# Optimization experiments

Hardware: AMD Instinct MI355X
Metric: run time of the kernel (lower is better)

The kernel has to match this reference:

```python
import jax, jax.numpy as jnp
import numpy as np

HIDDEN = 256        # hidden width of the dynamics MLP
N_ODE_STEPS = 2     # fixed-step RK4 steps over t_sim = [0, 1] per block


def setup_inputs() -> dict:
    key = jax.random.key(0)
    ks = jax.random.split(key, 8)
    S, B, N, d, p, block = 2, 8, 2048, 64, 32, 8
    s = jax.random.normal(ks[0], (S, B, N, d), jnp.float32)
    # strictly increasing time grid so delta = diff(t) > 0
    dt_raw = jax.random.uniform(ks[1], (S, B, block + 1), jnp.float32)
    t = jnp.cumsum(0.05 + 0.1 * dt_raw, axis=2)
    Phi = jax.random.normal(ks[2], (S, B, N, p), jnp.float32)
    b = 0.1 * jax.random.normal(ks[3], (S, B, N, d), jnp.float32)
    W1 = jax.random.normal(ks[4], (d + p, HIDDEN), jnp.float32) / np.sqrt(d + p).astype(np.float32)
    b1 = jnp.zeros((HIDDEN,), jnp.float32)
    W2 = jax.random.normal(ks[5], (HIDDEN, d), jnp.float32) / np.sqrt(HIDDEN).astype(np.float32)
    b2 = jnp.zeros((d,), jnp.float32)
    return dict(s=s, t=t, Phi=Phi, b=b, W1=W1, b1=b1, W2=W2, b2=b2)


def _dyn(x, Phi, b, W1, b1, W2, b2):
    # f(t, x, Phi, b): MLP over per-node latent + spatial features, plus forcing b.
    h = jnp.tanh(jnp.einsum('sbnf,fh->sbnh', jnp.concatenate([x, Phi], axis=-1), W1) + b1)
    return jnp.einsum('sbnh,hd->sbnd', h, W2) + b2 + b


def reference(s, t, Phi, b, W1, b1, W2, b2):
    S, B, N, d = s.shape
    block = t.shape[2] - 1
    delta = jnp.diff(t, axis=2)                      # (S, B, block)
    deltas = jnp.moveaxis(delta, 2, 0)[..., None, None]  # (block, S, B, 1, 1)
    dt = 1.0 / N_ODE_STEPS

    def g(x, dlt):
        # scaled dynamics: f(t, x, Phi, b) * delta  (time-rescaled to [0, 1])
        return _dyn(x, Phi, b, W1, b1, W2, b2) * dlt

    def block_step(x, dlt):
        def rk4(x, _):
            k1 = g(x, dlt)
            k2 = g(x + 0.5 * dt * k1, dlt)
            k3 = g(x + 0.5 * dt * k2, dlt)
            k4 = g(x + dt * k3, dlt)
            return x + (dt / 6.0) * (k1 + 2.0 * k2 + 2.0 * k3 + k4), None
        x, _ = jax.lax.scan(rk4, x, None, length=N_ODE_STEPS)
        return x, x

    _, s_stack = jax.lax.scan(block_step, s, deltas)  # (block, S, B, N, d)
    # 'S B block N d -> S (B block) N d'
    return jnp.moveaxis(s_stack, 0, 2).reshape(S, B * block, N, d)
```

## Files before the change

### kernel.cpp

```cpp
#include <hip/hip_runtime.h>

typedef short  short8   __attribute__((ext_vector_type(8)));
typedef float  floatx4  __attribute__((ext_vector_type(4)));
typedef unsigned int uintx2 __attribute__((ext_vector_type(2)));

#define LOG2E_X2 2.8853900817779268f

__device__ __forceinline__ float tanh_pre(float y) {
    float e = __builtin_amdgcn_exp2f(y);
    return 1.0f - 2.0f * __builtin_amdgcn_rcpf(1.0f + e);
}

__device__ __forceinline__ unsigned short bf16rne(float f) {
    unsigned u = __float_as_uint(f);
    u += 0x7FFFu + ((u >> 16) & 1u);
    return (unsigned short)(u >> 16);
}

#if __has_builtin(__builtin_amdgcn_cvt_pk_bf16_f32)
__device__ __forceinline__ unsigned pk2(float a, float b) {
    auto r = __builtin_amdgcn_cvt_pk_bf16_f32(a, b);
    unsigned u; __builtin_memcpy(&u, &r, 4);
    return u;
}
#else
__device__ __forceinline__ unsigned pk2(float a, float b) {
    unsigned r;
    asm("v_cvt_pk_bf16_f32 %0, %1, %2" : "=v"(r) : "v"(a), "v"(b));
    return r;
}
#endif

__global__ __launch_bounds__(512, 4) void ode_mfma(
    const float* __restrict__ s_in,  const float* __restrict__ t_in,
    const float* __restrict__ phi_in,const float* __restrict__ bfr_in,
    const float* __restrict__ w1_in, const float* __restrict__ b1_in,
    const float* __restrict__ w2_in, const float* __restrict__ b2_in,
    float* __restrict__ out)
{
    const int tid  = threadIdx.x;
    const int w    = tid >> 6;
    const int wv2  = w & 3;
    const int rh   = w >> 2;
    const int lane = tid & 63;
    const int l15  = lane & 15;
    const int q    = lane >> 4;
    const int wg   = blockIdx.x;
    const int sb   = wg >> 5;
    const int n0   = (wg & 31) << 6;
    const int rowg0 = sb * 2048 + n0;

    __shared__ __align__(16) unsigned short Atile[64][104];
    __shared__ __align__(16) unsigned short Hs[64][264];
    __shared__ __align__(16) float b1s[256];
    __shared__ float dls[8];

    const int d0 = wv2 * 16 + q * 4;

    short8 w1f[2][3];
#pragma unroll
    for (int ht = 0; ht < 2; ++ht)
#pragma unroll
        for (int kk = 0; kk < 3; ++kk) {
            short8 f;
#pragma unroll
            for (int j = 0; j < 8; ++j) {
                int k = kk * 32 + q * 8 + j;
                int hc = w * 32 + ht * 16 + l15;
                f[j] = (short)bf16rne(w1_in[k * 256 + hc] * LOG2E_X2);
            }
            w1f[ht][kk] = f;
        }
    short8 w2f[8];
#pragma unroll
    for (int kk = 0; kk < 8; ++kk) {
        short8 f;
#pragma unroll
        for (int j = 0; j < 8; ++j) {
            int k = kk * 32 + q * 8 + j;
            f[j] = (short)bf16rne(w2_in[k * 64 + wv2 * 16 + l15]);
        }
        w2f[kk] = f;
    }

    floatx4 xv[2], kacc[2], fbv[2];
    {
        const floatx4 b2v = *(const floatx4*)(b2_in + d0);
#pragma unroll
        for (int si = 0; si < 2; ++si) {
            int rt = si * 2 + rh;
            int rg = rowg0 + rt * 16 + l15;
            xv[si]  = *(const floatx4*)(s_in   + rg * 64 + d0);
            fbv[si] = b2v + *(const floatx4*)(bfr_in + rg * 64 + d0);
            uintx2 px = { pk2(xv[si][0], xv[si][1]), pk2(xv[si][2], xv[si][3]) };
            *(uintx2*)&Atile[rt * 16 + l15][d0] = px;
        }
    }
    {
        int row = tid >> 3, cc = tid & 7;
        floatx4 p = *(const floatx4*)(phi_in + (rowg0 + row) * 32 + cc * 4);
        uintx2 px = { pk2(p[0], p[1]), pk2(p[2], p[3]) };
        *(uintx2*)&Atile[row][64 + cc * 4] = px;
    }
    if (tid < 64) {
        floatx4 v = *(const floatx4*)(b1_in + tid * 4);
        v *= LOG2E_X2;
        *(floatx4*)&b1s[tid * 4] = v;
    }
    if (tid < 8)  dls[tid] = t_in[sb * 9 + tid + 1] - t_in[sb * 9 + tid];

    __syncthreads();

#define DO_G1(RT0)                                                              \
    {                                                                           \
        floatx4 acc1[2][2];                                                     \
        {                                                                       \
            short8 xb[2];                                                       \
            _Pragma("unroll")                                                   \
            for (int r2 = 0; r2 < 2; ++r2)                                      \
                xb[r2] = *(const short8*)&Atile[(RT0 + r2) * 16 + l15][q * 8];  \
            _Pragma("unroll")                                                   \
            for (int ht = 0; ht < 2; ++ht) {                                    \
                floatx4 bbf = *(const floatx4*)&b1s[w * 32 + ht * 16 + q * 4];  \
                _Pragma("unroll")                                               \
                for (int r2 = 0; r2 < 2; ++r2)                                  \
                    acc1[ht][r2] = __builtin_amdgcn_mfma_f32_16x16x32_bf16(     \
                        w1f[ht][0], xb[r2], bbf, 0, 0, 0);                      \
            }                                                                   \
        }                                                                       \
        _Pragma("unroll")                                                       \
        for (int kk = 1; kk < 3; ++kk) {                                        \
            short8 xb[2];                                                       \
            _Pragma("unroll")                                                   \
            for (int r2 = 0; r2 < 2; ++r2)                                      \
                xb[r2] = *(const short8*)&Atile[(RT0 + r2) * 16 + l15][kk * 32 + q * 8]; \
            _Pragma("unroll")                                                   \
            for (int ht = 0; ht < 2; ++ht)                                      \
                _Pragma("unroll")                                               \
                for (int r2 = 0; r2 < 2; ++r2)                                  \
                    acc1[ht][r2] = __builtin_amdgcn_mfma_f32_16x16x32_bf16(     \
                        w1f[ht][kk], xb[r2], acc1[ht][r2], 0, 0, 0);            \
        }                                                                       \
        _Pragma("unroll")                                                       \
        for (int ht = 0; ht < 2; ++ht)                                          \
            _Pragma("unroll")                                                   \
            for (int r2 = 0; r2 < 2; ++r2) {                                    \
                uintx2 hp = { pk2(tanh_pre(acc1[ht][r2][0]), tanh_pre(acc1[ht][r2][1])), \
                              pk2(tanh_pre(acc1[ht][r2][2]), tanh_pre(acc1[ht][r2][3])) }; \
                *(uintx2*)&Hs[(RT0 + r2) * 16 + l15][w * 32 + ht * 16 + q * 4] = hp; \
            }                                                                   \
    }

#define DO_G2(SI)                                                               \
    {                                                                           \
        const int rt = (SI) * 2 + rh;                                           \
        floatx4 acc2;                                                           \
        {                                                                       \
            short8 hb = *(const short8*)&Hs[rt * 16 + l15][q * 8];              \
            acc2 = __builtin_amdgcn_mfma_f32_16x16x32_bf16(                     \
                w2f[0], hb, fbv[SI], 0, 0, 0);                                  \
        }                                                                       \
        _Pragma("unroll")                                                       \
        for (int kk = 1; kk < 8; ++kk) {                                        \
            short8 hb = *(const short8*)&Hs[rt * 16 + l15][kk * 32 + q * 8];    \
            acc2 = __builtin_amdgcn_mfma_f32_16x16x32_bf16(                     \
                w2f[kk], hb, acc2, 0, 0, 0);                                    \
        }                                                                       \
        {                                                                       \
            floatx4 kv = acc2 * dlt;                                            \
            floatx4 xe;                                                         \
            if (sub == 0)      { kacc[SI] = kv;            xe = xv[SI] + 0.25f * kv; } \
            else if (sub == 1) { kacc[SI] += 2.0f * kv;    xe = xv[SI] + 0.25f * kv; } \
            else if (sub == 2) { kacc[SI] += 2.0f * kv;    xe = xv[SI] + 0.5f  * kv; } \
            else               { xv[SI] += (kacc[SI] + kv) * (1.0f / 12.0f); xe = xv[SI]; } \
            uintx2 px = { pk2(xe[0], xe[1]), pk2(xe[2], xe[3]) };               \
            *(uintx2*)&Atile[rt * 16 + l15][d0] = px;                           \
        }                                                                       \
        if ((i & 7) == 7) {                                                     \
            const int ob = (sb * 8 + (i >> 3)) * 2048;                          \
            *(floatx4*)(out + (size_t)(ob + n0 + rt * 16 + l15) * 64 + d0) = xv[SI]; \
        }                                                                       \
    }

    DO_G1(0)

#pragma unroll 1
    for (int i = 0; i < 64; ++i) {
        const float dlt = dls[i >> 3];
        const int sub = i & 3;
        __syncthreads();
        DO_G2(0)
        DO_G1(2)
        __syncthreads();
        DO_G2(1)
        if (i < 63) { DO_G1(0) }
    }
#undef DO_G1
#undef DO_G2
}

extern "C" void kernel_launch(void* const* d_in, const int* in_sizes, int n_in,
                              void* d_out, int out_size, void* d_ws, size_t ws_size,
                              hipStream_t stream) {
    const float* s_in  = (const float*)d_in[0];
    const float* t_in  = (const float*)d_in[1];
    const float* phi   = (const float*)d_in[2];
    const float* bfr   = (const float*)d_in[3];
    const float* w1    = (const float*)d_in[4];
    const float* b1    = (const float*)d_in[5];
    const float* w2    = (const float*)d_in[6];
    const float* b2    = (const float*)d_in[7];
    ode_mfma<<<512, 512, 0, stream>>>(s_in, t_in, phi, bfr, w1, b1, w2, b2, (float*)d_out);
}
```

Baseline: 337.8 us.

## Specialize warps into layer-1 producers and layer-2 consumers with register-resident weights

Splits the eight waves into two roles. Four waves run only the first MLP layer with tanh, holding four hidden tiles of W1 and b1 in registers. The other four run only the second layer and the RK4 update, holding W2 and the state. The forcing term is stored packed as bf16 to save registers. The aim is to pipeline the two layers across wave groups so MFMA and transcendental work overlap. In exchange the load balance between the groups is uneven and the forcing add loses precision.

```diff
diff --git a/kernel.cpp b/kernel.cpp
--- a/kernel.cpp
+++ b/kernel.cpp
@@ -30,6 +30,15 @@
     return r;
 }
 #endif
+
+__device__ __forceinline__ floatx4 unpk4(uintx2 u) {
+    floatx4 r;
+    r[0] = __uint_as_float(u.x << 16);
+    r[1] = __uint_as_float(u.x & 0xffff0000u);
+    r[2] = __uint_as_float(u.y << 16);
+    r[3] = __uint_as_float(u.y & 0xffff0000u);
+    return r;
+}
 
 __global__ __launch_bounds__(512, 4) void ode_mfma(
     const float* __restrict__ s_in,  const float* __restrict__ t_in,
@@ -40,8 +49,6 @@
 {
     const int tid  = threadIdx.x;
     const int w    = tid >> 6;
-    const int wv2  = w & 3;
-    const int rh   = w >> 2;
     const int lane = tid & 63;
     const int l15  = lane & 15;
     const int q    = lane >> 4;
@@ -52,81 +59,30 @@
 
     __shared__ __align__(16) unsigned short Atile[64][104];
     __shared__ __align__(16) unsigned short Hs[64][264];
-    __shared__ __align__(16) float b1s[256];
     __shared__ float dls[8];
 
-    const int d0 = wv2 * 16 + q * 4;
-
-    short8 w1f[2][3];
-#pragma unroll
-    for (int ht = 0; ht < 2; ++ht)
-#pragma unroll
-        for (int kk = 0; kk < 3; ++kk) {
-            short8 f;
-#pragma unroll
-            for (int j = 0; j < 8; ++j) {
-                int k = kk * 32 + q * 8 + j;
-                int hc = w * 32 + ht * 16 + l15;
-                f[j] = (short)bf16rne(w1_in[k * 256 + hc] * LOG2E_X2);
-            }
-            w1f[ht][kk] = f;
-        }
-    short8 w2f[8];
-#pragma unroll
-    for (int kk = 0; kk < 8; ++kk) {
-        short8 f;
-#pragma unroll
-        for (int j = 0; j < 8; ++j) {
-            int k = kk * 32 + q * 8 + j;
-            f[j] = (short)bf16rne(w2_in[k * 64 + wv2 * 16 + l15]);
-        }
-        w2f[kk] = f;
-    }
-
-    floatx4 xv[2], kacc[2], fbv[2];
-    {
-        const floatx4 b2v = *(const floatx4*)(b2_in + d0);
-#pragma unroll
-        for (int si = 0; si < 2; ++si) {
-            int rt = si * 2 + rh;
-            int rg = rowg0 + rt * 16 + l15;
-            xv[si]  = *(const floatx4*)(s_in   + rg * 64 + d0);
-            fbv[si] = b2v + *(const floatx4*)(bfr_in + rg * 64 + d0);
-            uintx2 px = { pk2(xv[si][0], xv[si][1]), pk2(xv[si][2], xv[si][3]) };
-            *(uintx2*)&Atile[rt * 16 + l15][d0] = px;
-        }
-    }
     {
         int row = tid >> 3, cc = tid & 7;
         floatx4 p = *(const floatx4*)(phi_in + (rowg0 + row) * 32 + cc * 4);
         uintx2 px = { pk2(p[0], p[1]), pk2(p[2], p[3]) };
         *(uintx2*)&Atile[row][64 + cc * 4] = px;
     }
-    if (tid < 64) {
-        floatx4 v = *(const floatx4*)(b1_in + tid * 4);
-        v *= LOG2E_X2;
-        *(floatx4*)&b1s[tid * 4] = v;
-    }
-    if (tid < 8)  dls[tid] = t_in[sb * 9 + tid + 1] - t_in[sb * 9 + tid];
-
-    __syncthreads();
+    if (tid < 8) dls[tid] = t_in[sb * 9 + tid + 1] - t_in[sb * 9 + tid];
 
 #define DO_G1(RT0)                                                              \
     {                                                                           \
-        floatx4 acc1[2][2];                                                     \
+        floatx4 acc1[4][2];                                                     \
         {                                                                       \
             short8 xb[2];                                                       \
             _Pragma("unroll")                                                   \
             for (int r2 = 0; r2 < 2; ++r2)                                      \
                 xb[r2] = *(const short8*)&Atile[(RT0 + r2) * 16 + l15][q * 8];  \
             _Pragma("unroll")                                                   \
-            for (int ht = 0; ht < 2; ++ht) {                                    \
-                floatx4 bbf = *(const floatx4*)&b1s[w * 32 + ht * 16 + q * 4];  \
+            for (int ht = 0; ht < 4; ++ht)                                      \
                 _Pragma("unroll")                                               \
                 for (int r2 = 0; r2 < 2; ++r2)                                  \
                     acc1[ht][r2] = __builtin_amdgcn_mfma_f32_16x16x32_bf16(     \
-                        w1f[ht][0], xb[r2], bbf, 0, 0, 0);                      \
-            }                                                                   \
+                        w1f[ht][0], xb[r2], bbf[ht], 0, 0, 0);                  \
         }                                                                       \
         _Pragma("unroll")                                                       \
         for (int kk = 1; kk < 3; ++kk) {                                        \
@@ -135,65 +91,143 @@
             for (int r2 = 0; r2 < 2; ++r2)                                      \
                 xb[r2] = *(const short8*)&Atile[(RT0 + r2) * 16 + l15][kk * 32 + q * 8]; \
             _Pragma("unroll")                                                   \
-            for (int ht = 0; ht < 2; ++ht)                                      \
+            for (int ht = 0; ht < 4; ++ht)                                      \
                 _Pragma("unroll")                                               \
                 for (int r2 = 0; r2 < 2; ++r2)                                  \
                     acc1[ht][r2] = __builtin_amdgcn_mfma_f32_16x16x32_bf16(     \
                         w1f[ht][kk], xb[r2], acc1[ht][r2], 0, 0, 0);            \
         }                                                                       \
         _Pragma("unroll")                                                       \
-        for (int ht = 0; ht < 2; ++ht)                                          \
+        for (int ht = 0; ht < 4; ++ht)                                          \
             _Pragma("unroll")                                                   \
             for (int r2 = 0; r2 < 2; ++r2) {                                    \
                 uintx2 hp = { pk2(tanh_pre(acc1[ht][r2][0]), tanh_pre(acc1[ht][r2][1])), \
                               pk2(tanh_pre(acc1[ht][r2][2]), tanh_pre(acc1[ht][r2][3])) }; \
-                *(uintx2*)&Hs[(RT0 + r2) * 16 + l15][w * 32 + ht * 16 + q * 4] = hp; \
+                *(uintx2*)&Hs[(RT0 + r2) * 16 + l15][hb0 + ht * 16 + q * 4] = hp; \
             }                                                                   \
     }
 
 #define DO_G2(SI)                                                               \
     {                                                                           \
-        const int rt = (SI) * 2 + rh;                                           \
-        floatx4 acc2;                                                           \
+        const int rt = (SI) * 2 + rt_rel;                                       \
+        const unsigned short* hrow = &Hs[rt * 16 + l15][0];                     \
+        floatx4 acc2a, acc2b;                                                   \
         {                                                                       \
-            short8 hb = *(const short8*)&Hs[rt * 16 + l15][q * 8];              \
-            acc2 = __builtin_amdgcn_mfma_f32_16x16x32_bf16(                     \
-                w2f[0], hb, fbv[SI], 0, 0, 0);                                  \
+            short8 hb = *(const short8*)&hrow[q * 8];                           \
+            acc2a = __builtin_amdgcn_mfma_f32_16x16x32_bf16(                    \
+                w2f[0][0], hb, unpk4(fpk[SI][0]), 0, 0, 0);                     \
+            acc2b = __builtin_amdgcn_mfma_f32_16x16x32_bf16(                    \
+                w2f[1][0], hb, unpk4(fpk[SI][1]), 0, 0, 0);                     \
         }                                                                       \
         _Pragma("unroll")                                                       \
         for (int kk = 1; kk < 8; ++kk) {                                        \
-            short8 hb = *(const short8*)&Hs[rt * 16 + l15][kk * 32 + q * 8];    \
-            acc2 = __builtin_amdgcn_mfma_f32_16x16x32_bf16(                     \
-                w2f[kk], hb, acc2, 0, 0, 0);                                    \
-        }                                                                       \
-        {                                                                       \
-            floatx4 kv = acc2 * dlt;                                            \
+            short8 hb = *(const short8*)&hrow[kk * 32 + q * 8];                 \
+            acc2a = __builtin_amdgcn_mfma_f32_16x16x32_bf16(                    \
+                w2f[0][kk], hb, acc2a, 0, 0, 0);                                \
+            acc2b = __builtin_amdgcn_mfma_f32_16x16x32_bf16(                    \
+                w2f[1][kk], hb, acc2b, 0, 0, 0);                                \
+        }                                                                       \
+        _Pragma("unroll")                                                       \
+        for (int h = 0; h < 2; ++h) {                                           \
+            floatx4 kv = (h == 0 ? acc2a : acc2b) * dlt;                        \
             floatx4 xe;                                                         \
-            if (sub == 0)      { kacc[SI] = kv;            xe = xv[SI] + 0.25f * kv; } \
-            else if (sub == 1) { kacc[SI] += 2.0f * kv;    xe = xv[SI] + 0.25f * kv; } \
-            else if (sub == 2) { kacc[SI] += 2.0f * kv;    xe = xv[SI] + 0.5f  * kv; } \
-            else               { xv[SI] += (kacc[SI] + kv) * (1.0f / 12.0f); xe = xv[SI]; } \
+            if (sub == 0)      { kacc[SI][h] = kv;            xe = xv[SI][h] + 0.25f * kv; } \
+            else if (sub == 1) { kacc[SI][h] += 2.0f * kv;    xe = xv[SI][h] + 0.25f * kv; } \
+            else if (sub == 2) { kacc[SI][h] += 2.0f * kv;    xe = xv[SI][h] + 0.5f  * kv; } \
+            else               { xv[SI][h] += (kacc[SI][h] + kv) * (1.0f / 12.0f); xe = xv[SI][h]; } \
             uintx2 px = { pk2(xe[0], xe[1]), pk2(xe[2], xe[3]) };               \
-            *(uintx2*)&Atile[rt * 16 + l15][d0] = px;                           \
-        }                                                                       \
-        if ((i & 7) == 7) {                                                     \
-            const int ob = (sb * 8 + (i >> 3)) * 2048;                          \
-            *(floatx4*)(out + (size_t)(ob + n0 + rt * 16 + l15) * 64 + d0) = xv[SI]; \
-        }                                                                       \
-    }
-
-    DO_G1(0)
-
+            *(uintx2*)&Atile[rt * 16 + l15][dp + h * 16 + q * 4] = px;          \
+        }                                                                       \
+        if (ii == 7) {                                                          \
+            const size_t ob = (size_t)((sb * 8 + blk) * 2048 + n0 + rt * 16 + l15) * 64; \
+            _Pragma("unroll")                                                   \
+            for (int h = 0; h < 2; ++h)                                         \
+                *(floatx4*)(out + ob + dp + h * 16 + q * 4) = xv[SI][h];        \
+        }                                                                       \
+    }
+
+    if (w < 4) {
+        const int hb0 = w * 64;
+        short8 w1f[4][3];
+#pragma unroll
+        for (int ht = 0; ht < 4; ++ht)
+#pragma unroll
+            for (int kk = 0; kk < 3; ++kk) {
+                short8 f;
+#pragma unroll
+                for (int j = 0; j < 8; ++j) {
+                    int k = kk * 32 + q * 8 + j;
+                    int hc = hb0 + ht * 16 + l15;
+                    f[j] = (short)bf16rne(w1_in[k * 256 + hc] * LOG2E_X2);
+                }
+                w1f[ht][kk] = f;
+            }
+        floatx4 bbf[4];
+#pragma unroll
+        for (int ht = 0; ht < 4; ++ht) {
+            floatx4 v = *(const floatx4*)(b1_in + hb0 + ht * 16 + q * 4);
+            bbf[ht] = v * LOG2E_X2;
+        }
+
+        __syncthreads();
+        DO_G1(0)
 #pragma unroll 1
-    for (int i = 0; i < 64; ++i) {
-        const float dlt = dls[i >> 3];
-        const int sub = i & 3;
+        for (int it = 0; it < 64; ++it) {
+            __syncthreads();
+            DO_G1(2)
+            __syncthreads();
+            if (it < 63) { DO_G1(0) }
+        }
+    } else {
+        const int g = w - 4;
+        const int rt_rel = g >> 1;
+        const int dp = (g & 1) * 32;
+        short8 w2f[2][8];
+#pragma unroll
+        for (int h = 0; h < 2; ++h)
+#pragma unroll
+            for (int kk = 0; kk < 8; ++kk) {
+                short8 f;
+#pragma unroll
+                for (int j = 0; j < 8; ++j) {
+                    int k = kk * 32 + q * 8 + j;
+                    f[j] = (short)bf16rne(w2_in[k * 64 + dp + h * 16 + l15]);
+                }
+                w2f[h][kk] = f;
+            }
+
+        floatx4 xv[2][2], kacc[2][2];
+        uintx2 fpk[2][2];
+#pragma unroll
+        for (int si = 0; si < 2; ++si) {
+            const int rt = si * 2 + rt_rel;
+            const int rg = rowg0 + rt * 16 + l15;
+#pragma unroll
+            for (int h = 0; h < 2; ++h) {
+                const int dh = dp + h * 16 + q * 4;
+                xv[si][h] = *(const floatx4*)(s_in + rg * 64 + dh);
+                floatx4 fb = *(const floatx4*)(b2_in + dh)
+                           + *(const floatx4*)(bfr_in + rg * 64 + dh);
+                fpk[si][h] = (uintx2){ pk2(fb[0], fb[1]), pk2(fb[2], fb[3]) };
+                uintx2 px = { pk2(xv[si][h][0], xv[si][h][1]),
+                              pk2(xv[si][h][2], xv[si][h][3]) };
+                *(uintx2*)&Atile[rt * 16 + l15][dh] = px;
+            }
+        }
+
         __syncthreads();
-        DO_G2(0)
-        DO_G1(2)
-        __syncthreads();
-        DO_G2(1)
-        if (i < 63) { DO_G1(0) }
+#pragma unroll 1
+        for (int blk = 0; blk < 8; ++blk) {
+            const float dlt = dls[blk];
+#pragma unroll 1
+            for (int ii = 0; ii < 8; ++ii) {
+                const int sub = ii & 3;
+                __syncthreads();
+                DO_G2(0)
+                __syncthreads();
+                DO_G2(1)
+            }
+        }
     }
 #undef DO_G1
 #undef DO_G2
```

Measured after the change: 298.3 us. 11.7% less time.
